# Kernel optimization log

Measured on AMD Instinct MI355X. Metric: run time of the kernel, lower is better.

Reference implementation:

```python
import jax, jax.numpy as jnp
import numpy as np

DIM = 768
N_HEADS = 12
HEAD_DIM = DIM // N_HEADS
HIDDEN = 4 * DIM
EPS = 1e-5


def _layernorm(x, gamma, beta):
    mu = jnp.mean(x, axis=-1, keepdims=True)
    var = jnp.mean(jnp.square(x - mu), axis=-1, keepdims=True)
    return (x - mu) * jax.lax.rsqrt(var + EPS) * gamma + beta


def setup_inputs() -> dict:
    key = jax.random.key(0)
    ks = jax.random.split(key, 8)
    B, N = 16, 1024
    s = 0.02
    return {
        "x": jax.random.normal(ks[0], (B, N, DIM), jnp.float32),
        "Wqkv": jax.random.normal(ks[1], (DIM, 3 * DIM), jnp.float32) * s,
        "bqkv": jnp.zeros((3 * DIM,), jnp.float32),
        "Wproj": jax.random.normal(ks[2], (DIM, DIM), jnp.float32) * s,
        "bproj": jnp.zeros((DIM,), jnp.float32),
        "g1": jnp.ones((DIM,), jnp.float32),
        "b1": jnp.zeros((DIM,), jnp.float32),
        "g2": jnp.ones((DIM,), jnp.float32),
        "b2": jnp.zeros((DIM,), jnp.float32),
        "W1": jax.random.normal(ks[3], (DIM, HIDDEN), jnp.float32) * s,
        "bf1": jnp.zeros((HIDDEN,), jnp.float32),
        "W2": jax.random.normal(ks[4], (HIDDEN, DIM), jnp.float32) * s,
        "bf2": jnp.zeros((DIM,), jnp.float32),
    }


def reference(x, Wqkv, bqkv, Wproj, bproj, g1, b1, g2, b2, W1, bf1, W2, bf2):
    B, N, _ = x.shape
    # --- attention branch (pre-LN) ---
    h = _layernorm(x, g1, b1)
    qkv = (h @ Wqkv + bqkv).reshape(B, N, 3, N_HEADS, HEAD_DIM)
    qkv = jnp.transpose(qkv, (2, 0, 3, 1, 4))  # [3, B, H, N, D]
    q, k, v = qkv[0], qkv[1], qkv[2]
    # NOTE: source scales by dim**-0.5, not head_dim**-0.5 (faithful)
    scores = jnp.einsum("bhnd,bhmd->bhnm", q, k) * (DIM ** -0.5)
    attn = jax.nn.softmax(scores, axis=-1)
    out = jnp.einsum("bhnm,bhmd->bhnd", attn, v)
    out = jnp.transpose(out, (0, 2, 1, 3)).reshape(B, N, DIM)
    x = x + (out @ Wproj + bproj)
    # --- MLP branch ---
    h2 = _layernorm(x, g2, b2)
    ff = jax.nn.relu(h2 @ W1 + bf1) @ W2 + bf2
    return x + ff
```

## Files before the change

kernel.cpp:

```cpp
#include <hip/hip_runtime.h>
#include <cstdint>
#include <cstddef>

typedef unsigned short u16;
typedef __bf16 bf16x8 __attribute__((ext_vector_type(8)));
typedef unsigned short u16x8 __attribute__((ext_vector_type(8)));
typedef float f32x4 __attribute__((ext_vector_type(4)));

#define DIMN 768
#define BNROWS 16384
#define NH 12
#define HD 64
#define HID 3072
#define QKVN 2304

__device__ __forceinline__ u16 f2bf(float f) {
  unsigned u = __builtin_bit_cast(unsigned, f);
  u += 0x7fffu + ((u >> 16) & 1u);
  return (u16)(u >> 16);
}

__device__ __forceinline__ bf16x8 ld8(const u16* p) {
  u16x8 v = *reinterpret_cast<const u16x8*>(p);
  return __builtin_bit_cast(bf16x8, v);
}

__device__ __forceinline__ void gload16(const void* g, void* l) {
  __builtin_amdgcn_global_load_lds(
      (const __attribute__((address_space(1))) unsigned int*)g,
      (__attribute__((address_space(3))) unsigned int*)l, 16, 0, 0);
}

#define MFMA(a, b, c) __builtin_amdgcn_mfma_f32_16x16x32_bf16(a, b, c, 0, 0, 0)

__global__ __launch_bounds__(256) void twb4_k(const float* __restrict__ Wqkv,
                                              const float* __restrict__ Wproj,
                                              const float* __restrict__ W1,
                                              const float* __restrict__ W2,
                                              u16* __restrict__ WqkvT,
                                              u16* __restrict__ WprojT,
                                              u16* __restrict__ W1T,
                                              u16* __restrict__ W2T) {
  __shared__ float tile[32][33];
  int bid = blockIdx.x;
  const float* W;
  u16* Wt;
  int K, N, nx;
  if (bid < 1728) {
    W = Wqkv; Wt = WqkvT; K = DIMN; N = QKVN; nx = 72;
  } else if (bid < 1728 + 576) {
    bid -= 1728; W = Wproj; Wt = WprojT; K = DIMN; N = DIMN; nx = 24;
  } else if (bid < 1728 + 576 + 2304) {
    bid -= 1728 + 576; W = W1; Wt = W1T; K = DIMN; N = HID; nx = 96;
  } else {
    bid -= 1728 + 576 + 2304; W = W2; Wt = W2T; K = HID; N = DIMN; nx = 24;
  }
  const int n0 = (bid % nx) * 32, k0 = (bid / nx) * 32;
  const int tx = threadIdx.x & 31, ty = threadIdx.x >> 5;
#pragma unroll
  for (int i = 0; i < 4; i++)
    tile[ty + i * 8][tx] = W[(size_t)(k0 + ty + i * 8) * N + n0 + tx];
  __syncthreads();
#pragma unroll
  for (int i = 0; i < 4; i++)
    Wt[(size_t)(n0 + ty + i * 8) * K + k0 + tx] = f2bf(tile[tx][ty + i * 8]);
}

__global__ __launch_bounds__(256) void ln_k(const float* __restrict__ x,
                                            const float* __restrict__ g,
                                            const float* __restrict__ bta,
                                            u16* __restrict__ outp) {
  const int row = blockIdx.x * 4 + (threadIdx.x >> 6);
  const int lane = threadIdx.x & 63;
  const float4* xr = (const float4*)(x + (size_t)row * DIMN);
  float4 v[3];
  float s = 0.f, ss = 0.f;
#pragma unroll
  for (int c = 0; c < 3; c++) {
    v[c] = xr[c * 64 + lane];
    s += v[c].x + v[c].y + v[c].z + v[c].w;
    ss += v[c].x * v[c].x + v[c].y * v[c].y + v[c].z * v[c].z + v[c].w * v[c].w;
  }
#pragma unroll
  for (int off = 1; off < 64; off <<= 1) {
    s += __shfl_xor(s, off);
    ss += __shfl_xor(ss, off);
  }
  const float mu = s * (1.f / DIMN);
  const float var = ss * (1.f / DIMN) - mu * mu;
  const float rs = rsqrtf(var + 1e-5f);
  u16* orow = outp + (size_t)row * DIMN;
#pragma unroll
  for (int c = 0; c < 3; c++) {
    float4 gv = ((const float4*)g)[c * 64 + lane];
    float4 bv = ((const float4*)bta)[c * 64 + lane];
    ushort4 o;
    o.x = f2bf((v[c].x - mu) * rs * gv.x + bv.x);
    o.y = f2bf((v[c].y - mu) * rs * gv.y + bv.y);
    o.z = f2bf((v[c].z - mu) * rs * gv.z + bv.z);
    o.w = f2bf((v[c].w - mu) * rs * gv.w + bv.w);
    ((ushort4*)orow)[c * 64 + lane] = o;
  }
}

template <int OUT_BF16, int RELU, int RESID>
__global__ __launch_bounds__(512, 2) void gemm256_k(const u16* __restrict__ A,
                                                    const u16* __restrict__ Bt,
                                                    const float* __restrict__ bias,
                                                    const float* __restrict__ resid,
                                                    void* __restrict__ Cout, int N, int K) {
  __shared__ u16 lds[65536];
  const int tid = threadIdx.x;
  const int m0 = blockIdx.x * 256;
  const int n0 = blockIdx.y * 256;
  const int lane = tid & 63, w = tid >> 6;
  const int wr = w >> 2, wc = w & 3;
  const int lhi = lane >> 4, llo = lane & 15;
  const int rdoff = (lhi ^ ((llo >> 1) & 3)) * 16;
  const int NT = K >> 5;

  const int srow = tid >> 2;
  const int sc8 = ((tid & 3) ^ ((srow >> 1) & 3)) * 8;
  const u16* aS0 = A + (size_t)(m0 + srow) * K + sc8;
  const u16* aS1 = A + (size_t)(m0 + 128 + srow) * K + sc8;
  const u16* bS0 = Bt + (size_t)(n0 + srow) * K + sc8;
  const u16* bS1 = Bt + (size_t)(n0 + 128 + srow) * K + sc8;

  auto slotBase = [&](int t) -> const char* { return (const char*)lds + ((size_t)(t & 3) << 15); };
  auto stageA = [&](int t) {
    char* sb = (char*)lds + ((size_t)(t & 3) << 15);
    gload16(aS0 + t * 32, sb + tid * 16);
    gload16(aS1 + t * 32, sb + 8192 + tid * 16);
  };
  auto stageB = [&](int t) {
    char* sb = (char*)lds + ((size_t)(t & 3) << 15) + 16384;
    gload16(bS0 + t * 32, sb + tid * 16);
    gload16(bS1 + t * 32, sb + 8192 + tid * 16);
  };

  f32x4 acc[8][4] = {};
  bf16x8 a03[2][4], bfr[2][4], a47[4];

  stageB(0); stageA(0);
  stageB(1); stageA(1);
  stageB(2); stageA(2);
  asm volatile("s_waitcnt vmcnt(8)" ::: "memory");
  __builtin_amdgcn_s_barrier();
  {
    const char* sb = slotBase(0);
#pragma unroll
    for (int ni = 0; ni < 4; ni++)
      bfr[0][ni] = ld8((const u16*)(sb + 16384 + (wc * 64 + ni * 16 + llo) * 64 + rdoff));
#pragma unroll
    for (int mi = 0; mi < 4; mi++)
      a03[0][mi] = ld8((const u16*)(sb + (wr * 128 + mi * 16 + llo) * 64 + rdoff));
  }

#define G256_P1(T, CUR)                                                                  \
  {                                                                                      \
    const char* sbp = slotBase(T);                                                       \
    _Pragma("unroll") for (int mi = 0; mi < 4; mi++)                                     \
        a47[mi] = ld8((const u16*)(sbp + (wr * 128 + (4 + mi) * 16 + llo) * 64 + rdoff));\
    if ((T) + 3 < NT) stageB((T) + 3);                                                   \
    if ((T) + 3 < NT) {                                                                  \
      asm volatile("s_waitcnt vmcnt(6)" ::: "memory");                                   \
    } else if ((T) + 2 < NT) {                                                           \
      asm volatile("s_waitcnt vmcnt(4)" ::: "memory");                                   \
    } else if ((T) + 1 < NT) {                                                           \
      asm volatile("s_waitcnt vmcnt(0)" ::: "memory");                                   \
    }                                                                                    \
    __builtin_amdgcn_s_barrier();                                                        \
    asm volatile("s_waitcnt lgkmcnt(4)" ::: "memory");                                   \
    __builtin_amdgcn_sched_barrier(0);                                                   \
    __builtin_amdgcn_s_setprio(1);                                                       \
    _Pragma("unroll") for (int mi = 0; mi < 4; mi++)                                     \
        _Pragma("unroll") for (int ni = 0; ni < 4; ni++)                                 \
            acc[mi][ni] = MFMA(a03[CUR][mi], bfr[CUR][ni], acc[mi][ni]);                 \
    __builtin_amdgcn_s_setprio(0);                                                       \
    __builtin_amdgcn_sched_barrier(0);                                                   \
  }

#define G256_P2(T, CUR, NXT)                                                             \
  {                                                                                      \
    if ((T) + 1 < NT) {                                                                  \
      const char* sbn = slotBase((T) + 1);                                               \
      _Pragma("unroll") for (int ni = 0; ni < 4; ni++)                                   \
          bfr[NXT][ni] =                                                                 \
              ld8((const u16*)(sbn + 16384 + (wc * 64 + ni * 16 + llo) * 64 + rdoff));   \
      _Pragma("unroll") for (int mi = 0; mi < 4; mi++)                                   \
          a03[NXT][mi] = ld8((const u16*)(sbn + (wr * 128 + mi * 16 + llo) * 64 + rdoff));\
    }                                                                                    \
    if ((T) + 3 < NT) stageA((T) + 3);                                                   \
    __builtin_amdgcn_s_barrier();                                                        \
    if ((T) + 1 < NT) {                                                                  \
      asm volatile("s_waitcnt lgkmcnt(8)" ::: "memory");                                 \
    } else {                                                                             \
      asm volatile("s_waitcnt lgkmcnt(0)" ::: "memory");                                 \
    }                                                                                    \
    __builtin_amdgcn_sched_barrier(0);                                                   \
    __builtin_amdgcn_s_setprio(1);                                                       \
    _Pragma("unroll") for (int mi = 0; mi < 4; mi++)                                     \
        _Pragma("unroll") for (int ni = 0; ni < 4; ni++)                                 \
            acc[4 + mi][ni] = MFMA(a47[mi], bfr[CUR][ni], acc[4 + mi][ni]);              \
    __builtin_amdgcn_s_setprio(0);                                                       \
    __builtin_amdgcn_sched_barrier(0);                                                   \
  }

  for (int t = 0; t < NT; t += 2) {
    G256_P1(t, 0)
    G256_P2(t, 0, 1)
    G256_P1(t + 1, 1)
    G256_P2(t + 1, 1, 0)
  }
#undef G256_P1
#undef G256_P2

#pragma unroll
  for (int mi = 0; mi < 8; mi++)
#pragma unroll
    for (int ni = 0; ni < 4; ni++) {
      const int row = m0 + wr * 128 + mi * 16 + lhi * 4;
      const int col = n0 + wc * 64 + ni * 16 + llo;
      const float bsv = bias[col];
#pragma unroll
      for (int rr = 0; rr < 4; rr++) {
        float v = acc[mi][ni][rr] + bsv;
        if (RELU) v = fmaxf(v, 0.0f);
        const size_t idx = (size_t)(row + rr) * N + col;
        if (RESID) v += resid[idx];
        if (OUT_BF16)
          ((u16*)Cout)[idx] = f2bf(v);
        else
          ((float*)Cout)[idx] = v;
      }
    }
}

template <int OUT_BF16, int RELU, int RESID>
__global__ __launch_bounds__(256, 2) void gemmP_k(const u16* __restrict__ A,
                                                  const u16* __restrict__ Bt,
                                                  const float* __restrict__ bias,
                                                  const float* __restrict__ resid,
                                                  void* __restrict__ Cout, int N, int K) {
  __shared__ u16 lds[3 * 12288];
  const int tid = threadIdx.x;
  const int m0 = blockIdx.x * 256;
  const int n0 = blockIdx.y * 128;
  const int lane = tid & 63, w = tid >> 6;
  const int wr = w >> 1, wc = w & 1;
  const int lhi = lane >> 4, llo = lane & 15;
  const int rdoff = (lhi ^ ((llo >> 1) & 3)) * 16;
  const int NT = K >> 5;

  const int crow = tid >> 2;
  const int kc8 = ((tid & 3) ^ ((crow >> 1) & 3)) * 8;
  const u16* aS = A + (size_t)(m0 + crow) * K + kc8;
  const u16* bS = Bt + (size_t)(n0 + crow) * K + kc8;
  const size_t a64 = (size_t)64 * K;

  auto slotBase = [&](int t) -> const char* { return (const char*)lds + (size_t)(t % 3) * 24576; };
  auto stage1 = [&](int t) {
    char* sb = (char*)lds + (size_t)(t % 3) * 24576;
    gload16(aS + t * 32, sb + tid * 16);
    gload16(aS + a64 + t * 32, sb + 4096 + tid * 16);
    gload16(bS + t * 32, sb + 16384 + tid * 16);
  };
  auto stage2 = [&](int t) {
    char* sb = (char*)lds + (size_t)(t % 3) * 24576;
    gload16(aS + 2 * a64 + t * 32, sb + 8192 + tid * 16);
    gload16(aS + 3 * a64 + t * 32, sb + 12288 + tid * 16);
    gload16(bS + a64 + t * 32, sb + 16384 + 4096 + tid * 16);
  };

  f32x4 acc[8][4] = {};
  bf16x8 a03[2][4], bfr[2][4], a47[4];

  stage1(0); stage2(0);
  stage1(1); stage2(1);
  asm volatile("s_waitcnt vmcnt(6)" ::: "memory");
  __builtin_amdgcn_s_barrier();
  {
    const char* sb = slotBase(0);
#pragma unroll
    for (int ni = 0; ni < 4; ni++)
      bfr[0][ni] = ld8((const u16*)(sb + 16384 + (wc * 64 + ni * 16 + llo) * 64 + rdoff));
#pragma unroll
    for (int mi = 0; mi < 4; mi++)
      a03[0][mi] = ld8((const u16*)(sb + (wr * 128 + mi * 16 + llo) * 64 + rdoff));
  }

#define GP_P1(T, CUR)                                                                    \
  {                                                                                      \
    const char* sbp = slotBase(T);                                                       \
    _Pragma("unroll") for (int mi = 0; mi < 4; mi++)                                     \
        a47[mi] = ld8((const u16*)(sbp + (wr * 128 + (4 + mi) * 16 + llo) * 64 + rdoff));\
    if ((T) + 2 < NT) stage1((T) + 2);                                                   \
    if ((T) + 2 < NT) {                                                                  \
      asm volatile("s_waitcnt vmcnt(3)" ::: "memory");                                   \
    } else if ((T) + 1 < NT) {                                                           \
      asm volatile("s_waitcnt vmcnt(0)" ::: "memory");                                   \
    }                                                                                    \
    __builtin_amdgcn_s_barrier();                                                        \
    asm volatile("s_waitcnt lgkmcnt(4)" ::: "memory");                                   \
    __builtin_amdgcn_sched_barrier(0);                                                   \
    __builtin_amdgcn_s_setprio(1);                                                       \
    _Pragma("unroll") for (int mi = 0; mi < 4; mi++)                                     \
        _Pragma("unroll") for (int ni = 0; ni < 4; ni++)                                 \
            acc[mi][ni] = MFMA(a03[CUR][mi], bfr[CUR][ni], acc[mi][ni]);                 \
    __builtin_amdgcn_s_setprio(0);                                                       \
    __builtin_amdgcn_sched_barrier(0);                                                   \
  }

#define GP_P2(T, CUR, NXT)                                                               \
  {                                                                                      \
    if ((T) + 1 < NT) {                                                                  \
      const char* sbn = slotBase((T) + 1);                                               \
      _Pragma("unroll") for (int ni = 0; ni < 4; ni++)                                   \
          bfr[NXT][ni] =                                                                 \
              ld8((const u16*)(sbn + 16384 + (wc * 64 + ni * 16 + llo) * 64 + rdoff));   \
      _Pragma("unroll") for (int mi = 0; mi < 4; mi++)                                   \
          a03[NXT][mi] = ld8((const u16*)(sbn + (wr * 128 + mi * 16 + llo) * 64 + rdoff));\
    }                                                                                    \
    if ((T) + 2 < NT) stage2((T) + 2);                                                   \
    __builtin_amdgcn_s_barrier();                                                        \
    if ((T) + 1 < NT) {                                                                  \
      asm volatile("s_waitcnt lgkmcnt(8)" ::: "memory");                                 \
    } else {                                                                             \
      asm volatile("s_waitcnt lgkmcnt(0)" ::: "memory");                                 \
    }                                                                                    \
    __builtin_amdgcn_sched_barrier(0);                                                   \
    __builtin_amdgcn_s_setprio(1);                                                       \
    _Pragma("unroll") for (int mi = 0; mi < 4; mi++)                                     \
        _Pragma("unroll") for (int ni = 0; ni < 4; ni++)                                 \
            acc[4 + mi][ni] = MFMA(a47[mi], bfr[CUR][ni], acc[4 + mi][ni]);              \
    __builtin_amdgcn_s_setprio(0);                                                       \
    __builtin_amdgcn_sched_barrier(0);                                                   \
  }

  for (int t = 0; t < NT; t += 2) {
    GP_P1(t, 0)
    GP_P2(t, 0, 1)
    GP_P1(t + 1, 1)
    GP_P2(t + 1, 1, 0)
  }
#undef GP_P1
#undef GP_P2

#pragma unroll
  for (int mi = 0; mi < 8; mi++)
#pragma unroll
    for (int ni = 0; ni < 4; ni++) {
      const int row = m0 + wr * 128 + mi * 16 + lhi * 4;
      const int col = n0 + wc * 64 + ni * 16 + llo;
      const float bsv = bias[col];
#pragma unroll
      for (int rr = 0; rr < 4; rr++) {
        float v = acc[mi][ni][rr] + bsv;
        if (RELU) v = fmaxf(v, 0.0f);
        const size_t idx = (size_t)(row + rr) * N + col;
        if (RESID) v += resid[idx];
        if (OUT_BF16)
          ((u16*)Cout)[idx] = f2bf(v);
        else
          ((float*)Cout)[idx] = v;
      }
    }
}

__device__ __forceinline__ bf16x8 ldscale8(const u16* p, float c) {
  u16x8 v = *reinterpret_cast<const u16x8*>(p);
  bf16x8 r;
#pragma unroll
  for (int j = 0; j < 8; j++) {
    float f = __builtin_bit_cast(float, (unsigned)v[j] << 16) * c;
    r[j] = (__bf16)f;
  }
  return r;
}

__device__ __forceinline__ unsigned pack_bf2(float a, float b) {
  unsigned ua = (unsigned)__builtin_bit_cast(u16, (__bf16)a);
  unsigned ub = (unsigned)__builtin_bit_cast(u16, (__bf16)b);
  return ua | (ub << 16);
}

__global__ __launch_bounds__(256, 3) void attn_k(const u16* __restrict__ qkv,
                                                 u16* __restrict__ outp) {
  __shared__ u16 Ks[2][64 * 64];
  __shared__ u16 Vt[2][64 * 64];
  __shared__ u16 Ps[4][32 * 64];

  const int tid = threadIdx.x;
  const int f = blockIdx.x;
  const int bh = (f & 7) | ((f >> 6) << 3);
  const int qt = (f >> 3) & 7;
  const int b = bh / NH, h = bh - b * NH;
  const int lane = tid & 63, w = tid >> 6;
  const int lhi = lane >> 4, llo = lane & 15;
  const size_t rowb = (size_t)b * 1024;
  const int wq0 = qt * 128 + w * 32;
  const float SC = 0.052059750f;

  bf16x8 qb[2][2];
#pragma unroll
  for (int mi = 0; mi < 2; mi++) {
    const u16* qrow = qkv + (rowb + wq0 + mi * 16 + llo) * QKVN + h * HD;
    qb[mi][0] = ldscale8(qrow + lhi * 8, SC);
    qb[mi][1] = ldscale8(qrow + 32 + lhi * 8, SC);
  }

  bf16x8 ones;
#pragma unroll
  for (int j = 0; j < 8; j++) ones[j] = (__bf16)1.0f;

  const u16* kbase = qkv + rowb * QKVN + DIMN + h * HD;
  const u16* vbase = qkv + rowb * QKVN + 2 * DIMN + h * HD;
  const int sw = (llo & 7) * 8;
  const int rsw = llo & 7;

  const int srow = tid >> 3, su = tid & 7;
  const u16* ksrc = kbase + (size_t)srow * QKVN + (su ^ (srow & 7)) * 8;
  auto stageK = [&](int kt, int slot) {
    const u16* s0 = ksrc + (size_t)kt * 64 * QKVN;
    gload16(s0, (char*)&Ks[slot][0] + tid * 16);
    gload16(s0 + (size_t)32 * QKVN, (char*)&Ks[slot][0] + 4096 + tid * 16);
  };

  const int vp = (lane & 31) * 2;
  const int dc = w * 8 + (lane >> 5) * 32;
  auto loadV = [&](int kt, u16x8& a, u16x8& c) {
    const u16* vr = vbase + (size_t)(kt * 64 + vp) * QKVN + dc;
    a = *reinterpret_cast<const u16x8*>(vr);
    c = *reinterpret_cast<const u16x8*>(vr + QKVN);
  };
  auto writeV = [&](int buf, u16x8 a, u16x8 c) {
#pragma unroll
    for (int j = 0; j < 8; j++) {
      unsigned val = (unsigned)a[j] | ((unsigned)c[j] << 16);
      *reinterpret_cast<unsigned*>(&Vt[buf][(dc + j) * 64 + (vp ^ (j * 8))]) = val;
    }
  };

  u16x8 v0, v1, nv0, nv1;

  stageK(0, 0);
  loadV(0, v0, v1);
  stageK(1, 1);
  asm volatile("s_waitcnt vmcnt(2)" ::: "memory");
  writeV(0, v0, v1);
  asm volatile("s_waitcnt lgkmcnt(0)" ::: "memory");
  __builtin_amdgcn_s_barrier();
  __builtin_amdgcn_sched_barrier(0);

  f32x4 oacc[2][4] = {};
  f32x4 racc[2] = {};

  for (int t = 0; t < 16; t++) {
    if (t < 15) loadV(t + 1, nv0, nv1);

    const u16* kB = &Ks[t & 1][0];
    f32x4 sacc[4][2] = {};
#pragma unroll
    for (int ks = 0; ks < 2; ks++)
#pragma unroll
      for (int ni = 0; ni < 4; ni++) {
        bf16x8 kf = ld8(&kB[(ni * 16 + llo) * 64 + (((ks * 4 + lhi) ^ rsw) * 8)]);
#pragma unroll
        for (int mi = 0; mi < 2; mi++) sacc[ni][mi] = MFMA(kf, qb[mi][ks], sacc[ni][mi]);
      }

    asm volatile("s_waitcnt lgkmcnt(0)" ::: "memory");
    __builtin_amdgcn_s_barrier();
    __builtin_amdgcn_sched_barrier(0);
    if (t + 2 < 16) stageK(t + 2, t & 1);

#pragma unroll
    for (int mi = 0; mi < 2; mi++)
#pragma unroll
      for (int ni = 0; ni < 4; ni++) {
        float p0 = __builtin_amdgcn_exp2f(sacc[ni][mi][0]);
        float p1 = __builtin_amdgcn_exp2f(sacc[ni][mi][1]);
        float p2 = __builtin_amdgcn_exp2f(sacc[ni][mi][2]);
        float p3 = __builtin_amdgcn_exp2f(sacc[ni][mi][3]);
        u16* pp = &Ps[w][(mi * 16 + llo) * 64 + ((ni * 16 + lhi * 4) ^ sw)];
        uint2 pw;
        pw.x = pack_bf2(p0, p1);
        pw.y = pack_bf2(p2, p3);
        *reinterpret_cast<uint2*>(pp) = pw;
      }

#pragma unroll
    for (int ks = 0; ks < 2; ks++) {
      const int koff = ks * 32 + lhi * 8;
      bf16x8 pa0 = ld8(&Ps[w][llo * 64 + (koff ^ sw)]);
      bf16x8 pa1 = ld8(&Ps[w][(16 + llo) * 64 + (koff ^ sw)]);
#pragma unroll
      for (int ni = 0; ni < 4; ni++) {
        bf16x8 vb = ld8(&Vt[t & 1][(ni * 16 + llo) * 64 + (koff ^ sw)]);
        oacc[0][ni] = MFMA(pa0, vb, oacc[0][ni]);
        oacc[1][ni] = MFMA(pa1, vb, oacc[1][ni]);
      }
      racc[0] = MFMA(pa0, ones, racc[0]);
      racc[1] = MFMA(pa1, ones, racc[1]);
    }

    if (t < 15) {
      if (t + 2 < 16) {
        asm volatile("s_waitcnt vmcnt(2)" ::: "memory");
      } else {
        asm volatile("s_waitcnt vmcnt(0)" ::: "memory");
      }
      writeV((t + 1) & 1, nv0, nv1);
      v0 = nv0; v1 = nv1;
      asm volatile("s_waitcnt lgkmcnt(0)" ::: "memory");
      __builtin_amdgcn_s_barrier();
      __builtin_amdgcn_sched_barrier(0);
    }
  }

#pragma unroll
  for (int mi = 0; mi < 2; mi++)
#pragma unroll
    for (int ni = 0; ni < 4; ni++)
#pragma unroll
      for (int r = 0; r < 4; r++) {
        const size_t row = rowb + wq0 + mi * 16 + lhi * 4 + r;
        outp[row * DIMN + h * HD + ni * 16 + llo] = f2bf(oacc[mi][ni][r] / racc[mi][r]);
      }
}

extern "C" void kernel_launch(void* const* d_in, const int* in_sizes, int n_in,
                              void* d_out, int out_size, void* d_ws, size_t ws_size,
                              hipStream_t stream) {
  const float* x = (const float*)d_in[0];
  const float* Wqkv = (const float*)d_in[1];
  const float* bqkv = (const float*)d_in[2];
  const float* Wproj = (const float*)d_in[3];
  const float* bproj = (const float*)d_in[4];
  const float* g1 = (const float*)d_in[5];
  const float* b1 = (const float*)d_in[6];
  const float* g2 = (const float*)d_in[7];
  const float* b2 = (const float*)d_in[8];
  const float* W1 = (const float*)d_in[9];
  const float* bf1 = (const float*)d_in[10];
  const float* W2 = (const float*)d_in[11];
  const float* bf2 = (const float*)d_in[12];
  float* outp = (float*)d_out;

  char* p = (char*)d_ws;
  u16* WqkvT = (u16*)p; p += (size_t)QKVN * DIMN * 2;
  u16* WprojT = (u16*)p; p += (size_t)DIMN * DIMN * 2;
  u16* W1T = (u16*)p; p += (size_t)HID * DIMN * 2;
  u16* W2T = (u16*)p; p += (size_t)DIMN * HID * 2;
  u16* bufX = (u16*)p; p += (size_t)BNROWS * DIMN * 2;
  u16* big = (u16*)p; p += (size_t)BNROWS * HID * 2;

  twb4_k<<<6912, 256, 0, stream>>>(Wqkv, Wproj, W1, W2, WqkvT, WprojT, W1T, W2T);

  ln_k<<<BNROWS / 4, 256, 0, stream>>>(x, g1, b1, bufX);
  gemm256_k<1, 0, 0><<<dim3(64, QKVN / 256), 512, 0, stream>>>(bufX, WqkvT, bqkv, nullptr,
                                                               big, QKVN, DIMN);
  attn_k<<<1536, 256, 0, stream>>>(big, bufX);
  gemmP_k<0, 0, 1><<<dim3(64, DIMN / 128), 256, 0, stream>>>(bufX, WprojT, bproj, x, outp,
                                                             DIMN, DIMN);
  ln_k<<<BNROWS / 4, 256, 0, stream>>>(outp, g2, b2, bufX);
  gemm256_k<1, 1, 0><<<dim3(64, HID / 256), 512, 0, stream>>>(bufX, W1T, bf1, nullptr, big,
                                                              HID, DIMN);
  gemmP_k<0, 0, 1><<<dim3(64, DIMN / 128), 256, 0, stream>>>(big, W2T, bf2, outp, outp,
                                                             DIMN, HID);
}
```

Before: 418.8 us.

## Shrink projection and MLP-down GEMM tiles to 128x128 with simpler pipeline

Replaces the 256x128 tile GEMM used for the output projection and the second MLP matmul with a 128x128 tile kernel. It has a single-stage-per-iteration triple-buffered loop and occupancy hint raised to 3. This doubles the grid from 384 to 768 blocks so the N=768 GEMMs fill the 256 CUs better. The cost is lower operand reuse per block and the loss of the split-phase LDS/MFMA overlap, since the loop now waits on all LDS reads before its MFMAs.

Result: slower. 430.0 us (+2.7%).

```diff
diff --git a/kernel.cpp b/kernel.cpp
--- a/kernel.cpp
+++ b/kernel.cpp
@@ -237,14 +237,14 @@
 }
 
 template <int OUT_BF16, int RELU, int RESID>
-__global__ __launch_bounds__(256, 2) void gemmP_k(const u16* __restrict__ A,
-                                                  const u16* __restrict__ Bt,
-                                                  const float* __restrict__ bias,
-                                                  const float* __restrict__ resid,
-                                                  void* __restrict__ Cout, int N, int K) {
-  __shared__ u16 lds[3 * 12288];
+__global__ __launch_bounds__(256, 3) void gemmP128_k(const u16* __restrict__ A,
+                                                     const u16* __restrict__ Bt,
+                                                     const float* __restrict__ bias,
+                                                     const float* __restrict__ resid,
+                                                     void* __restrict__ Cout, int N, int K) {
+  __shared__ u16 lds[3 * 8192];
   const int tid = threadIdx.x;
-  const int m0 = blockIdx.x * 256;
+  const int m0 = blockIdx.x * 128;
   const int n0 = blockIdx.y * 128;
   const int lane = tid & 63, w = tid >> 6;
   const int wr = w >> 1, wc = w & 1;
@@ -258,99 +258,54 @@
   const u16* bS = Bt + (size_t)(n0 + crow) * K + kc8;
   const size_t a64 = (size_t)64 * K;
 
-  auto slotBase = [&](int t) -> const char* { return (const char*)lds + (size_t)(t % 3) * 24576; };
-  auto stage1 = [&](int t) {
-    char* sb = (char*)lds + (size_t)(t % 3) * 24576;
+  auto slotBase = [&](int t) -> const char* { return (const char*)lds + (size_t)(t % 3) * 16384; };
+  auto stageAll = [&](int t) {
+    char* sb = (char*)lds + (size_t)(t % 3) * 16384;
     gload16(aS + t * 32, sb + tid * 16);
     gload16(aS + a64 + t * 32, sb + 4096 + tid * 16);
-    gload16(bS + t * 32, sb + 16384 + tid * 16);
+    gload16(bS + t * 32, sb + 8192 + tid * 16);
+    gload16(bS + a64 + t * 32, sb + 8192 + 4096 + tid * 16);
   };
-  auto stage2 = [&](int t) {
-    char* sb = (char*)lds + (size_t)(t % 3) * 24576;
-    gload16(aS + 2 * a64 + t * 32, sb + 8192 + tid * 16);
-    gload16(aS + 3 * a64 + t * 32, sb + 12288 + tid * 16);
-    gload16(bS + a64 + t * 32, sb + 16384 + 4096 + tid * 16);
-  };
-
-  f32x4 acc[8][4] = {};
-  bf16x8 a03[2][4], bfr[2][4], a47[4];
-
-  stage1(0); stage2(0);
-  stage1(1); stage2(1);
-  asm volatile("s_waitcnt vmcnt(6)" ::: "memory");
+
+  f32x4 acc[4][4] = {};
+  bf16x8 af[4], bfr[4];
+
+  stageAll(0);
+  stageAll(1);
+  asm volatile("s_waitcnt vmcnt(4)" ::: "memory");
   __builtin_amdgcn_s_barrier();
-  {
-    const char* sb = slotBase(0);
+
+  for (int t = 0; t < NT; ++t) {
+    const char* sb = slotBase(t);
 #pragma unroll
     for (int ni = 0; ni < 4; ni++)
-      bfr[0][ni] = ld8((const u16*)(sb + 16384 + (wc * 64 + ni * 16 + llo) * 64 + rdoff));
+      bfr[ni] = ld8((const u16*)(sb + 8192 + (wc * 64 + ni * 16 + llo) * 64 + rdoff));
 #pragma unroll
     for (int mi = 0; mi < 4; mi++)
-      a03[0][mi] = ld8((const u16*)(sb + (wr * 128 + mi * 16 + llo) * 64 + rdoff));
-  }
-
-#define GP_P1(T, CUR)                                                                    \
-  {                                                                                      \
-    const char* sbp = slotBase(T);                                                       \
-    _Pragma("unroll") for (int mi = 0; mi < 4; mi++)                                     \
-        a47[mi] = ld8((const u16*)(sbp + (wr * 128 + (4 + mi) * 16 + llo) * 64 + rdoff));\
-    if ((T) + 2 < NT) stage1((T) + 2);                                                   \
-    if ((T) + 2 < NT) {                                                                  \
-      asm volatile("s_waitcnt vmcnt(3)" ::: "memory");                                   \
-    } else if ((T) + 1 < NT) {                                                           \
-      asm volatile("s_waitcnt vmcnt(0)" ::: "memory");                                   \
-    }                                                                                    \
-    __builtin_amdgcn_s_barrier();                                                        \
-    asm volatile("s_waitcnt lgkmcnt(4)" ::: "memory");                                   \
-    __builtin_amdgcn_sched_barrier(0);                                                   \
-    __builtin_amdgcn_s_setprio(1);                                                       \
-    _Pragma("unroll") for (int mi = 0; mi < 4; mi++)                                     \
-        _Pragma("unroll") for (int ni = 0; ni < 4; ni++)                                 \
-            acc[mi][ni] = MFMA(a03[CUR][mi], bfr[CUR][ni], acc[mi][ni]);                 \
-    __builtin_amdgcn_s_setprio(0);                                                       \
-    __builtin_amdgcn_sched_barrier(0);                                                   \
-  }
-
-#define GP_P2(T, CUR, NXT)                                                               \
-  {                                                                                      \
-    if ((T) + 1 < NT) {                                                                  \
-      const char* sbn = slotBase((T) + 1);                                               \
-      _Pragma("unroll") for (int ni = 0; ni < 4; ni++)                                   \
-          bfr[NXT][ni] =                                                                 \
-              ld8((const u16*)(sbn + 16384 + (wc * 64 + ni * 16 + llo) * 64 + rdoff));   \
-      _Pragma("unroll") for (int mi = 0; mi < 4; mi++)                                   \
-          a03[NXT][mi] = ld8((const u16*)(sbn + (wr * 128 + mi * 16 + llo) * 64 + rdoff));\
-    }                                                                                    \
-    if ((T) + 2 < NT) stage2((T) + 2);                                                   \
-    __builtin_amdgcn_s_barrier();                                                        \
-    if ((T) + 1 < NT) {                                                                  \
-      asm volatile("s_waitcnt lgkmcnt(8)" ::: "memory");                                 \
-    } else {                                                                             \
-      asm volatile("s_waitcnt lgkmcnt(0)" ::: "memory");                                 \
-    }                                                                                    \
-    __builtin_amdgcn_sched_barrier(0);                                                   \
-    __builtin_amdgcn_s_setprio(1);                                                       \
-    _Pragma("unroll") for (int mi = 0; mi < 4; mi++)                                     \
-        _Pragma("unroll") for (int ni = 0; ni < 4; ni++)                                 \
-            acc[4 + mi][ni] = MFMA(a47[mi], bfr[CUR][ni], acc[4 + mi][ni]);              \
-    __builtin_amdgcn_s_setprio(0);                                                       \
-    __builtin_amdgcn_sched_barrier(0);                                                   \
-  }
-
-  for (int t = 0; t < NT; t += 2) {
-    GP_P1(t, 0)
-    GP_P2(t, 0, 1)
-    GP_P1(t + 1, 1)
-    GP_P2(t + 1, 1, 0)
-  }
-#undef GP_P1
-#undef GP_P2
-
-#pragma unroll
-  for (int mi = 0; mi < 8; mi++)
+      af[mi] = ld8((const u16*)(sb + (wr * 64 + mi * 16 + llo) * 64 + rdoff));
+    if (t + 2 < NT) stageAll(t + 2);
+    asm volatile("s_waitcnt lgkmcnt(0)" ::: "memory");
+    __builtin_amdgcn_sched_barrier(0);
+    __builtin_amdgcn_s_setprio(1);
+#pragma unroll
+    for (int mi = 0; mi < 4; mi++)
+#pragma unroll
+      for (int ni = 0; ni < 4; ni++) acc[mi][ni] = MFMA(af[mi], bfr[ni], acc[mi][ni]);
+    __builtin_amdgcn_s_setprio(0);
+    __builtin_amdgcn_sched_barrier(0);
+    if (t + 2 < NT) {
+      asm volatile("s_waitcnt vmcnt(4)" ::: "memory");
+    } else if (t + 1 < NT) {
+      asm volatile("s_waitcnt vmcnt(0)" ::: "memory");
+    }
+    __builtin_amdgcn_s_barrier();
+  }
+
+#pragma unroll
+  for (int mi = 0; mi < 4; mi++)
 #pragma unroll
     for (int ni = 0; ni < 4; ni++) {
-      const int row = m0 + wr * 128 + mi * 16 + lhi * 4;
+      const int row = m0 + wr * 64 + mi * 16 + lhi * 4;
       const int col = n0 + wc * 64 + ni * 16 + llo;
       const float bsv = bias[col];
 #pragma unroll
@@ -561,11 +516,11 @@
   gemm256_k<1, 0, 0><<<dim3(64, QKVN / 256), 512, 0, stream>>>(bufX, WqkvT, bqkv, nullptr,
                                                                big, QKVN, DIMN);
   attn_k<<<1536, 256, 0, stream>>>(big, bufX);
-  gemmP_k<0, 0, 1><<<dim3(64, DIMN / 128), 256, 0, stream>>>(bufX, WprojT, bproj, x, outp,
-                                                             DIMN, DIMN);
+  gemmP128_k<0, 0, 1><<<dim3(128, DIMN / 128), 256, 0, stream>>>(bufX, WprojT, bproj, x,
+                                                                 outp, DIMN, DIMN);
   ln_k<<<BNROWS / 4, 256, 0, stream>>>(outp, g2, b2, bufX);
   gemm256_k<1, 1, 0><<<dim3(64, HID / 256), 512, 0, stream>>>(bufX, W1T, bf1, nullptr, big,
                                                               HID, DIMN);
-  gemmP_k<0, 0, 1><<<dim3(64, DIMN / 128), 256, 0, stream>>>(big, W2T, bf2, outp, outp,
-                                                             DIMN, HID);
-}
+  gemmP128_k<0, 0, 1><<<dim3(128, DIMN / 128), 256, 0, stream>>>(big, W2T, bf2, outp, outp,
+                                                                 DIMN, HID);
+}
```
